# Optimization experiments

Hardware: AMD Instinct MI355X
Metric: run time of the kernel (lower is better)

Reference implementation:

```python
import jax, jax.numpy as jnp
import numpy as np

SOBEL_X = jnp.array([[-1., 0., 1.], [-2., 0., 2.], [-1., 0., 1.]], dtype=jnp.float32)
SOBEL_Y = jnp.array([[-1., -2., -1.], [0., 0., 0.], [1., 2., 1.]], dtype=jnp.float32)


def _dwconv(x, k):
    # depthwise 3x3 conv, padding=1, groups=C. x: [B,C,H,W], k: [3,3]
    C = x.shape[1]
    kern = jnp.broadcast_to(k[None, None], (C, 1, 3, 3)).astype(x.dtype)
    return jax.lax.conv_general_dilated(
        x, kern, window_strides=(1, 1), padding=((1, 1), (1, 1)),
        dimension_numbers=('NCHW', 'OIHW', 'NCHW'), feature_group_count=C)


def setup_inputs() -> dict:
    key = jax.random.key(0)
    k1, _ = jax.random.split(key)
    u = jax.random.normal(k1, (16, 3, 512, 512), dtype=jnp.float32)
    theta = jnp.ones((1,), dtype=jnp.float32)
    return {"u": u, "theta": theta}


def reference(u, theta):
    # first derivatives
    ux = _dwconv(u, SOBEL_X)
    uy = _dwconv(u, SOBEL_Y)
    # second derivatives
    uxx = _dwconv(ux, SOBEL_X)
    uxy = _dwconv(ux, SOBEL_Y)
    uyy = _dwconv(uy, SOBEL_Y)
    # Gaussian curvature
    denom = (1.0 + ux * ux + uy * uy) ** 2
    G = (uxx * uyy - uxy * uxy) / (denom + 1e-6)
    # theta * u is computed but unused in the original forward (kept faithful)
    _ = theta * u
    phi_G = jnp.exp(-jnp.abs(G))
    P = phi_G * ux
    Q = phi_G * uy
    div_term = _dwconv(P, SOBEL_X) + _dwconv(Q, SOBEL_Y)
    return u + div_term
```

## Files before the change

kernel.cpp:

```cpp
#include <hip/hip_runtime.h>
#include <math.h>


#define HB   16
#define NROW (HB + 6)
#define NT   256

#define STEP(TT, S0, S1, S2) do {                                              \
    const int Tt = (TT);                                                       \
      \
    float ur0 = ucen[S0][0], ur1 = ucen[S0][1],                                \
          ur2 = ucen[S0][2], ur3 = ucen[S0][3];                                \
    if (Tt < NROW) {                                                           \
                        \
        const int gy = gy0 + Tt - 3;                                           \
        float* w = uw[S0];                                                     \
        if ((unsigned)gy < (unsigned)H) {                                      \
            const float* row = uc + (long)gy * W;                              \
            const float4 va = *(const float4*)(row + ca);                      \
            const float4 vb = *(const float4*)(row + c0);                      \
            const float4 vc = *(const float4*)(row + cc);                      \
            w[0] = inb0  ? va.x : 0.f;  w[1]  = inb1  ? va.y : 0.f;            \
            w[2] = inb2  ? va.z : 0.f;  w[3]  = inb3  ? va.w : 0.f;            \
            w[4] = vb.x;                w[5]  = vb.y;                          \
            w[6] = vb.z;                w[7]  = vb.w;                          \
            w[8] = inb8  ? vc.x : 0.f;  w[9]  = inb9  ? vc.y : 0.f;            \
            w[10] = inb10 ? vc.z : 0.f; w[11] = inb11 ? vc.w : 0.f;            \
        } else {                                                               \
            _Pragma("unroll") for (int i = 0; i < 12; ++i) w[i] = 0.f;         \
        }                                                                      \
        ucen[S0][0] = w[4]; ucen[S0][1] = w[5];                                \
        ucen[S0][2] = w[6]; ucen[S0][3] = w[7];                                \
    }                                                                          \
    if (Tt >= 2 && Tt < NROW) {                                                \
                 \
        float* xr = xw[S2]; float* yr = yw[S2];                                \
        const int gy = gy0 + Tt - 4;                                           \
        if ((unsigned)gy < (unsigned)H) {                                      \
            const float* a = uw[S1];                             \
            const float* m = uw[S2];                             \
            const float* b = uw[S0];                             \
            _Pragma("unroll") for (int c = 0; c < 8; ++c) {                    \
                const float A = a[c+1], B = a[c+2], C = b_ = a[c+3];           \
                const float D = m[c+1],             E = m[c+3];                \
                const float F = b[c+1], Gg = b[c+2], Hh = b[c+3];              \
                float x = (C - A) + 2.f*(E - D) + (Hh - F);                    \
                float y = (F + 2.f*Gg + Hh) - (A + 2.f*B + C);                 \
                xr[c] = mU[c+2] ? x : 0.f;                                     \
                yr[c] = mU[c+2] ? y : 0.f;                                     \
            }                                                                  \
        } else {                                                               \
            _Pragma("unroll") for (int c = 0; c < 8; ++c) { xr[c]=0.f; yr[c]=0.f; } \
        }                                                                      \
    }                                                                          \
    if (Tt >= 4 && Tt < NROW) {                                                \
                     \
        float* dp = dP[S1]; float* eq = eQ[S1];                                \
        const int gy = gy0 + Tt - 5;                                           \
        if ((unsigned)gy < (unsigned)H) {                                      \
            const float* xt = xw[S0];                         \
            const float* xm = xw[S1];                         \
            const float* xb = xw[S2];                         \
            const float* yt = yw[S0];                                          \
            const float* ym = yw[S1];                                          \
            const float* yb = yw[S2];                                          \
            float P[6], Q[6];                                                  \
            _Pragma("unroll") for (int c = 0; c < 6; ++c) {                    \
                const float xc = xm[c+1], yc = ym[c+1];                        \
                const float uxx = (xt[c+2]-xt[c]) + 2.f*(xm[c+2]-xm[c])        \
                                + (xb[c+2]-xb[c]);                             \
                const float uxy = (xb[c] + 2.f*xb[c+1] + xb[c+2])              \
                                - (xt[c] + 2.f*xt[c+1] + xt[c+2]);             \
                const float uyy = (yb[c] + 2.f*yb[c+1] + yb[c+2])              \
                                - (yt[c] + 2.f*yt[c+1] + yt[c+2]);             \
                const float den = 1.f + xc*xc + yc*yc;                         \
                const float Gv = (uxx*uyy - uxy*uxy)                           \
                               * __builtin_amdgcn_rcpf(den*den + 1e-6f);       \
                const float phi = __expf(-fabsf(Gv));                          \
                P[c] = mU[c+3] ? phi * xc : 0.f;                               \
                Q[c] = mU[c+3] ? phi * yc : 0.f;                               \
            }                                                                  \
            dp[0] = P[2]-P[0]; dp[1] = P[3]-P[1];                              \
            dp[2] = P[4]-P[2]; dp[3] = P[5]-P[3];                              \
            eq[0] = Q[0]+2.f*Q[1]+Q[2]; eq[1] = Q[1]+2.f*Q[2]+Q[3];            \
            eq[2] = Q[2]+2.f*Q[3]+Q[4]; eq[3] = Q[3]+2.f*Q[4]+Q[5];            \
        } else {                                                               \
            _Pragma("unroll") for (int c = 0; c < 4; ++c) { dp[c]=0.f; eq[c]=0.f; } \
        }                                                                      \
    }                                                                          \
    if (Tt >= 6 && Tt < NROW) {                                                \
          \
          \
        float o0 = ur0 + (dP[S2][0] + 2.f*dP[S0][0] + dP[S1][0])               \
                       + (eQ[S1][0] - eQ[S2][0]);                              \
        float o1 = ur1 + (dP[S2][1] + 2.f*dP[S0][1] + dP[S1][1])               \
                       + (eQ[S1][1] - eQ[S2][1]);                              \
        float o2 = ur2 + (dP[S2][2] + 2.f*dP[S0][2] + dP[S1][2])               \
                       + (eQ[S1][2] - eQ[S2][2]);                              \
        float o3 = ur3 + (dP[S2][3] + 2.f*dP[S0][3] + dP[S1][3])               \
                       + (eQ[S1][3] - eQ[S2][3]);                              \
        *(float4*)(oc + (long)(gy0 + Tt - 6) * W + c0) =                       \
            make_float4(o0, o1, o2, o3);                                       \
    }                                                                          \
} while (0)

__global__ __launch_bounds__(NT) void gcdd_sweep(
    const float* __restrict__ u, float* __restrict__ out, int H, int W)
{
    const int tid   = threadIdx.x;
    const int strip = tid & 127;
    const int band  = tid >> 7;
    const int c0    = strip * 4;
    const int gy0   = (blockIdx.y * 2 + band) * HB;
    const long chan = blockIdx.z;
    const float* __restrict__ uc = u + chan * (long)H * W;
    float* __restrict__ oc = out + chan * (long)H * W;

    const int ca = (c0 - 4 < 0) ? 0 : (c0 - 4);
    const int cc = (c0 + 4 > W - 4) ? (W - 4) : (c0 + 4);

    bool mU[12];
    #pragma unroll
    for (int i = 0; i < 12; ++i)
        mU[i] = (unsigned)(c0 - 4 + i) < (unsigned)W;
    const bool inb0 = mU[0], inb1 = mU[1], inb2 = mU[2], inb3 = mU[3];
    const bool inb8 = mU[8], inb9 = mU[9], inb10 = mU[10], inb11 = mU[11];

    float uw[3][12];
    float ucen[3][4] = {};
    float xw[3][8], yw[3][8];
    float dP[3][4], eQ[3][4];
    float b_;
    (void)b_;

    for (int t = 0; t < NROW + 2; t += 3) {
        STEP(t + 0, 0, 1, 2);
        STEP(t + 1, 1, 2, 0);
        STEP(t + 2, 2, 0, 1);
    }
}

extern "C" void kernel_launch(void* const* d_in, const int* in_sizes, int n_in,
                              void* d_out, int out_size, void* d_ws, size_t ws_size,
                              hipStream_t stream) {
    const float* u = (const float*)d_in[0];
    float* out = (float*)d_out;

    const int H = 512, W = 512;
    const int channels = in_sizes[0] / (H * W);

    dim3 grid(1, H / (2 * HB), channels);
    dim3 block(NT);
    gcdd_sweep<<<grid, block, 0, stream>>>(u, out, H, W);
}
```

Measured before the change: 48.33 us.

## Prefetch input rows one step ahead with 4-slot ring and nontemporal stores

Loads of input rows now run one step ahead through a four-slot register ring, with a prologue load before the loop. The loop is unrolled by 12 so every slot index stays a compile-time constant. The goal is to overlap global load latency with the stencil maths of the current row. Output stores become nontemporal to avoid polluting the cache. This costs more registers, which could reduce occupancy, and the much larger unrolled body.

```diff
diff --git a/kernel.cpp b/kernel.cpp
--- a/kernel.cpp
+++ b/kernel.cpp
@@ -6,15 +6,17 @@
 #define NROW (HB + 6)
 #define NT   256
 
-#define STEP(TT, S0, S1, S2) do {                                              \
+typedef float f4v __attribute__((ext_vector_type(4)));
+
+#define STEP(TT, LS, AT, AM, AB, XW, XT, XM, XB, PW, PT, PM, PB) do {          \
     const int Tt = (TT);                                                       \
       \
-    float ur0 = ucen[S0][0], ur1 = ucen[S0][1],                                \
-          ur2 = ucen[S0][2], ur3 = ucen[S0][3];                                \
-    if (Tt < NROW) {                                                           \
-                        \
-        const int gy = gy0 + Tt - 3;                                           \
-        float* w = uw[S0];                                                     \
+    const float ur0 = ucen[LS][0], ur1 = ucen[LS][1],                          \
+                ur2 = ucen[LS][2], ur3 = ucen[LS][3];                          \
+    if (Tt + 1 < NROW) {                                                       \
+                     \
+        const int gy = gy0 + Tt - 2;                                           \
+        float* w = uw[LS];                                                     \
         if ((unsigned)gy < (unsigned)H) {                                      \
             const float* row = uc + (long)gy * W;                              \
             const float4 va = *(const float4*)(row + ca);                      \
@@ -29,23 +31,23 @@
         } else {                                                               \
             _Pragma("unroll") for (int i = 0; i < 12; ++i) w[i] = 0.f;         \
         }                                                                      \
-        ucen[S0][0] = w[4]; ucen[S0][1] = w[5];                                \
-        ucen[S0][2] = w[6]; ucen[S0][3] = w[7];                                \
+        ucen[LS][0] = w[4]; ucen[LS][1] = w[5];                                \
+        ucen[LS][2] = w[6]; ucen[LS][3] = w[7];                                \
     }                                                                          \
     if (Tt >= 2 && Tt < NROW) {                                                \
                  \
-        float* xr = xw[S2]; float* yr = yw[S2];                                \
+        float* xr = xw[XW]; float* yr = yw[XW];                                \
         const int gy = gy0 + Tt - 4;                                           \
         if ((unsigned)gy < (unsigned)H) {                                      \
-            const float* a = uw[S1];                             \
-            const float* m = uw[S2];                             \
-            const float* b = uw[S0];                             \
+            const float* a = uw[AT];                             \
+            const float* m = uw[AM];                             \
+            const float* b = uw[AB];                             \
             _Pragma("unroll") for (int c = 0; c < 8; ++c) {                    \
-                const float A = a[c+1], B = a[c+2], C = b_ = a[c+3];           \
+                const float A = a[c+1], B = a[c+2], C = a[c+3];                \
                 const float D = m[c+1],             E = m[c+3];                \
                 const float F = b[c+1], Gg = b[c+2], Hh = b[c+3];              \
-                float x = (C - A) + 2.f*(E - D) + (Hh - F);                    \
-                float y = (F + 2.f*Gg + Hh) - (A + 2.f*B + C);                 \
+                const float x = (C - A) + 2.f*(E - D) + (Hh - F);              \
+                const float y = (F + 2.f*Gg + Hh) - (A + 2.f*B + C);           \
                 xr[c] = mU[c+2] ? x : 0.f;                                     \
                 yr[c] = mU[c+2] ? y : 0.f;                                     \
             }                                                                  \
@@ -55,15 +57,15 @@
     }                                                                          \
     if (Tt >= 4 && Tt < NROW) {                                                \
                      \
-        float* dp = dP[S1]; float* eq = eQ[S1];                                \
+        float* dp = dP[PW]; float* eq = eQ[PW];                                \
         const int gy = gy0 + Tt - 5;                                           \
         if ((unsigned)gy < (unsigned)H) {                                      \
-            const float* xt = xw[S0];                         \
-            const float* xm = xw[S1];                         \
-            const float* xb = xw[S2];                         \
-            const float* yt = yw[S0];                                          \
-            const float* ym = yw[S1];                                          \
-            const float* yb = yw[S2];                                          \
+            const float* xt = xw[XT];                         \
+            const float* xm = xw[XM];                         \
+            const float* xb = xw[XB];                         \
+            const float* yt = yw[XT];                                          \
+            const float* ym = yw[XM];                                          \
+            const float* yb = yw[XB];                                          \
             float P[6], Q[6];                                                  \
             _Pragma("unroll") for (int c = 0; c < 6; ++c) {                    \
                 const float xc = xm[c+1], yc = ym[c+1];                        \
@@ -89,18 +91,17 @@
         }                                                                      \
     }                                                                          \
     if (Tt >= 6 && Tt < NROW) {                                                \
-          \
-          \
-        float o0 = ur0 + (dP[S2][0] + 2.f*dP[S0][0] + dP[S1][0])               \
-                       + (eQ[S1][0] - eQ[S2][0]);                              \
-        float o1 = ur1 + (dP[S2][1] + 2.f*dP[S0][1] + dP[S1][1])               \
-                       + (eQ[S1][1] - eQ[S2][1]);                              \
-        float o2 = ur2 + (dP[S2][2] + 2.f*dP[S0][2] + dP[S1][2])               \
-                       + (eQ[S1][2] - eQ[S2][2]);                              \
-        float o3 = ur3 + (dP[S2][3] + 2.f*dP[S0][3] + dP[S1][3])               \
-                       + (eQ[S1][3] - eQ[S2][3]);                              \
-        *(float4*)(oc + (long)(gy0 + Tt - 6) * W + c0) =                       \
-            make_float4(o0, o1, o2, o3);                                       \
+         \
+        f4v o;                                                                 \
+        o.x = ur0 + (dP[PT][0] + 2.f*dP[PM][0] + dP[PB][0])                    \
+                  + (eQ[PB][0] - eQ[PT][0]);                                   \
+        o.y = ur1 + (dP[PT][1] + 2.f*dP[PM][1] + dP[PB][1])                    \
+                  + (eQ[PB][1] - eQ[PT][1]);                                   \
+        o.z = ur2 + (dP[PT][2] + 2.f*dP[PM][2] + dP[PB][2])                    \
+                  + (eQ[PB][2] - eQ[PT][2]);                                   \
+        o.w = ur3 + (dP[PT][3] + 2.f*dP[PM][3] + dP[PB][3])                    \
+                  + (eQ[PB][3] - eQ[PT][3]);                                   \
+        __builtin_nontemporal_store(o, (f4v*)(oc + (long)(gy0 + Tt - 6) * W + c0)); \
     }                                                                          \
 } while (0)
 
@@ -126,17 +127,46 @@
     const bool inb0 = mU[0], inb1 = mU[1], inb2 = mU[2], inb3 = mU[3];
     const bool inb8 = mU[8], inb9 = mU[9], inb10 = mU[10], inb11 = mU[11];
 
-    float uw[3][12];
-    float ucen[3][4] = {};
+    float uw[4][12];
+    float ucen[4][4] = {};
     float xw[3][8], yw[3][8];
     float dP[3][4], eQ[3][4];
-    float b_;
-    (void)b_;
 
-    for (int t = 0; t < NROW + 2; t += 3) {
-        STEP(t + 0, 0, 1, 2);
-        STEP(t + 1, 1, 2, 0);
-        STEP(t + 2, 2, 0, 1);
+    {
+        const int gy = gy0 - 3;
+        float* w = uw[0];
+        if ((unsigned)gy < (unsigned)H) {
+            const float* row = uc + (long)gy * W;
+            const float4 va = *(const float4*)(row + ca);
+            const float4 vb = *(const float4*)(row + c0);
+            const float4 vc = *(const float4*)(row + cc);
+            w[0] = inb0  ? va.x : 0.f;  w[1]  = inb1  ? va.y : 0.f;
+            w[2] = inb2  ? va.z : 0.f;  w[3]  = inb3  ? va.w : 0.f;
+            w[4] = vb.x;                w[5]  = vb.y;
+            w[6] = vb.z;                w[7]  = vb.w;
+            w[8] = inb8  ? vc.x : 0.f;  w[9]  = inb9  ? vc.y : 0.f;
+            w[10] = inb10 ? vc.z : 0.f; w[11] = inb11 ? vc.w : 0.f;
+        } else {
+            #pragma unroll
+            for (int i = 0; i < 12; ++i) w[i] = 0.f;
+        }
+        ucen[0][0] = w[4]; ucen[0][1] = w[5];
+        ucen[0][2] = w[6]; ucen[0][3] = w[7];
+    }
+
+    for (int t = 0; t < 24; t += 12) {
+        STEP(t + 0,  1, 2, 3, 0,  2, 0, 1, 2,  1, 2, 0, 1);
+        STEP(t + 1,  2, 3, 0, 1,  0, 1, 2, 0,  2, 0, 1, 2);
+        STEP(t + 2,  3, 0, 1, 2,  1, 2, 0, 1,  0, 1, 2, 0);
+        STEP(t + 3,  0, 1, 2, 3,  2, 0, 1, 2,  1, 2, 0, 1);
+        STEP(t + 4,  1, 2, 3, 0,  0, 1, 2, 0,  2, 0, 1, 2);
+        STEP(t + 5,  2, 3, 0, 1,  1, 2, 0, 1,  0, 1, 2, 0);
+        STEP(t + 6,  3, 0, 1, 2,  2, 0, 1, 2,  1, 2, 0, 1);
+        STEP(t + 7,  0, 1, 2, 3,  0, 1, 2, 0,  2, 0, 1, 2);
+        STEP(t + 8,  1, 2, 3, 0,  1, 2, 0, 1,  0, 1, 2, 0);
+        STEP(t + 9,  2, 3, 0, 1,  2, 0, 1, 2,  1, 2, 0, 1);
+        STEP(t + 10, 3, 0, 1, 2,  0, 1, 2, 0,  2, 0, 1, 2);
+        STEP(t + 11, 0, 1, 2, 3,  1, 2, 0, 1,  0, 1, 2, 0);
     }
 }
 
```

New measurement: 50.05 us. 3.6% more time.

## Prefetch next input row and precompute separable row sums for first Sobel

Applied to the files above, without the earlier changes.

Loads of the next input row are issued one step ahead into a pending buffer so global load latency overlaps with the current row's compute. The first-derivative Sobel is split into horizontal difference and smoothing sums per row, which are reused across three output rows, cutting redundant adds. The column mask on P/Q is dropped, and outputs are written with nontemporal stores. Register pressure rises from the extra Du/Su arrays and the prefetch buffer. Removing the mask may change border results if the later stage relies on zeroed out-of-range P/Q.

```diff
diff --git a/kernel.cpp b/kernel.cpp
--- a/kernel.cpp
+++ b/kernel.cpp
@@ -6,46 +6,49 @@
 #define NROW (HB + 6)
 #define NT   256
 
+typedef float f4v __attribute__((ext_vector_type(4)));
+
 #define STEP(TT, S0, S1, S2) do {                                              \
     const int Tt = (TT);                                                       \
-      \
-    float ur0 = ucen[S0][0], ur1 = ucen[S0][1],                                \
-          ur2 = ucen[S0][2], ur3 = ucen[S0][3];                                \
+    const float ur0 = ucen[S0][0], ur1 = ucen[S0][1],                          \
+                ur2 = ucen[S0][2], ur3 = ucen[S0][3];                          \
     if (Tt < NROW) {                                                           \
-                        \
-        const int gy = gy0 + Tt - 3;                                           \
-        float* w = uw[S0];                                                     \
+               \
+        float* du = Du[S0]; float* su = Su[S0];                                \
+        _Pragma("unroll") for (int c = 0; c < 8; ++c) {                        \
+            du[c] = pend[c+3] - pend[c+1];                                     \
+            su[c] = pend[c+1] + 2.f*pend[c+2] + pend[c+3];                     \
+        }                                                                      \
+        ucen[S0][0] = pend[4]; ucen[S0][1] = pend[5];                          \
+        ucen[S0][2] = pend[6]; ucen[S0][3] = pend[7];                          \
+    }                                                                          \
+    if (Tt + 1 < NROW) {                                                       \
+         \
+        const int gy = gy0 + Tt - 2;                                           \
         if ((unsigned)gy < (unsigned)H) {                                      \
             const float* row = uc + (long)gy * W;                              \
             const float4 va = *(const float4*)(row + ca);                      \
             const float4 vb = *(const float4*)(row + c0);                      \
             const float4 vc = *(const float4*)(row + cc);                      \
-            w[0] = inb0  ? va.x : 0.f;  w[1]  = inb1  ? va.y : 0.f;            \
-            w[2] = inb2  ? va.z : 0.f;  w[3]  = inb3  ? va.w : 0.f;            \
-            w[4] = vb.x;                w[5]  = vb.y;                          \
-            w[6] = vb.z;                w[7]  = vb.w;                          \
-            w[8] = inb8  ? vc.x : 0.f;  w[9]  = inb9  ? vc.y : 0.f;            \
-            w[10] = inb10 ? vc.z : 0.f; w[11] = inb11 ? vc.w : 0.f;            \
+            pend[0] = inb0  ? va.x : 0.f;  pend[1]  = inb1  ? va.y : 0.f;      \
+            pend[2] = inb2  ? va.z : 0.f;  pend[3]  = inb3  ? va.w : 0.f;      \
+            pend[4] = vb.x;                pend[5]  = vb.y;                    \
+            pend[6] = vb.z;                pend[7]  = vb.w;                    \
+            pend[8] = inb8  ? vc.x : 0.f;  pend[9]  = inb9  ? vc.y : 0.f;      \
+            pend[10] = inb10 ? vc.z : 0.f; pend[11] = inb11 ? vc.w : 0.f;      \
         } else {                                                               \
-            _Pragma("unroll") for (int i = 0; i < 12; ++i) w[i] = 0.f;         \
+            _Pragma("unroll") for (int i = 0; i < 12; ++i) pend[i] = 0.f;      \
         }                                                                      \
-        ucen[S0][0] = w[4]; ucen[S0][1] = w[5];                                \
-        ucen[S0][2] = w[6]; ucen[S0][3] = w[7];                                \
     }                                                                          \
     if (Tt >= 2 && Tt < NROW) {                                                \
-                 \
+         \
         float* xr = xw[S2]; float* yr = yw[S2];                                \
         const int gy = gy0 + Tt - 4;                                           \
         if ((unsigned)gy < (unsigned)H) {                                      \
-            const float* a = uw[S1];                             \
-            const float* m = uw[S2];                             \
-            const float* b = uw[S0];                             \
+                                     \
             _Pragma("unroll") for (int c = 0; c < 8; ++c) {                    \
-                const float A = a[c+1], B = a[c+2], C = b_ = a[c+3];           \
-                const float D = m[c+1],             E = m[c+3];                \
-                const float F = b[c+1], Gg = b[c+2], Hh = b[c+3];              \
-                float x = (C - A) + 2.f*(E - D) + (Hh - F);                    \
-                float y = (F + 2.f*Gg + Hh) - (A + 2.f*B + C);                 \
+                const float x = Du[S1][c] + 2.f*Du[S2][c] + Du[S0][c];         \
+                const float y = Su[S0][c] - Su[S1][c];                         \
                 xr[c] = mU[c+2] ? x : 0.f;                                     \
                 yr[c] = mU[c+2] ? y : 0.f;                                     \
             }                                                                  \
@@ -54,7 +57,7 @@
         }                                                                      \
     }                                                                          \
     if (Tt >= 4 && Tt < NROW) {                                                \
-                     \
+         \
         float* dp = dP[S1]; float* eq = eQ[S1];                                \
         const int gy = gy0 + Tt - 5;                                           \
         if ((unsigned)gy < (unsigned)H) {                                      \
@@ -77,8 +80,9 @@
                 const float Gv = (uxx*uyy - uxy*uxy)                           \
                                * __builtin_amdgcn_rcpf(den*den + 1e-6f);       \
                 const float phi = __expf(-fabsf(Gv));                          \
-                P[c] = mU[c+3] ? phi * xc : 0.f;                               \
-                Q[c] = mU[c+3] ? phi * yc : 0.f;                               \
+                   \
+                P[c] = phi * xc;                                               \
+                Q[c] = phi * yc;                                               \
             }                                                                  \
             dp[0] = P[2]-P[0]; dp[1] = P[3]-P[1];                              \
             dp[2] = P[4]-P[2]; dp[3] = P[5]-P[3];                              \
@@ -89,18 +93,18 @@
         }                                                                      \
     }                                                                          \
     if (Tt >= 6 && Tt < NROW) {                                                \
-          \
-          \
-        float o0 = ur0 + (dP[S2][0] + 2.f*dP[S0][0] + dP[S1][0])               \
-                       + (eQ[S1][0] - eQ[S2][0]);                              \
-        float o1 = ur1 + (dP[S2][1] + 2.f*dP[S0][1] + dP[S1][1])               \
-                       + (eQ[S1][1] - eQ[S2][1]);                              \
-        float o2 = ur2 + (dP[S2][2] + 2.f*dP[S0][2] + dP[S1][2])               \
-                       + (eQ[S1][2] - eQ[S2][2]);                              \
-        float o3 = ur3 + (dP[S2][3] + 2.f*dP[S0][3] + dP[S1][3])               \
-                       + (eQ[S1][3] - eQ[S2][3]);                              \
-        *(float4*)(oc + (long)(gy0 + Tt - 6) * W + c0) =                       \
-            make_float4(o0, o1, o2, o3);                                       \
+         \
+                  \
+        f4v o;                                                                 \
+        o.x = ur0 + (dP[S2][0] + 2.f*dP[S0][0] + dP[S1][0])                    \
+                  + (eQ[S1][0] - eQ[S2][0]);                                   \
+        o.y = ur1 + (dP[S2][1] + 2.f*dP[S0][1] + dP[S1][1])                    \
+                  + (eQ[S1][1] - eQ[S2][1]);                                   \
+        o.z = ur2 + (dP[S2][2] + 2.f*dP[S0][2] + dP[S1][2])                    \
+                  + (eQ[S1][2] - eQ[S2][2]);                                   \
+        o.w = ur3 + (dP[S2][3] + 2.f*dP[S0][3] + dP[S1][3])                    \
+                  + (eQ[S1][3] - eQ[S2][3]);                                   \
+        __builtin_nontemporal_store(o, (f4v*)(oc + (long)(gy0 + Tt - 6) * W + c0)); \
     }                                                                          \
 } while (0)
 
@@ -126,12 +130,30 @@
     const bool inb0 = mU[0], inb1 = mU[1], inb2 = mU[2], inb3 = mU[3];
     const bool inb8 = mU[8], inb9 = mU[9], inb10 = mU[10], inb11 = mU[11];
 
-    float uw[3][12];
+    float pend[12];
+    float Du[3][8], Su[3][8];
     float ucen[3][4] = {};
     float xw[3][8], yw[3][8];
     float dP[3][4], eQ[3][4];
-    float b_;
-    (void)b_;
+
+    {
+        const int gy = gy0 - 3;
+        if ((unsigned)gy < (unsigned)H) {
+            const float* row = uc + (long)gy * W;
+            const float4 va = *(const float4*)(row + ca);
+            const float4 vb = *(const float4*)(row + c0);
+            const float4 vc = *(const float4*)(row + cc);
+            pend[0] = inb0  ? va.x : 0.f;  pend[1]  = inb1  ? va.y : 0.f;
+            pend[2] = inb2  ? va.z : 0.f;  pend[3]  = inb3  ? va.w : 0.f;
+            pend[4] = vb.x;                pend[5]  = vb.y;
+            pend[6] = vb.z;                pend[7]  = vb.w;
+            pend[8] = inb8  ? vc.x : 0.f;  pend[9]  = inb9  ? vc.y : 0.f;
+            pend[10] = inb10 ? vc.z : 0.f; pend[11] = inb11 ? vc.w : 0.f;
+        } else {
+            #pragma unroll
+            for (int i = 0; i < 12; ++i) pend[i] = 0.f;
+        }
+    }
 
     for (int t = 0; t < NROW + 2; t += 3) {
         STEP(t + 0, 0, 1, 2);
```

Result: slower. 51.43 us (+6.4%).
